# Kernel optimization log

Measured on AMD Instinct MI355X. Metric: run time of the kernel, lower is better.

Reference implementation:

```python
import jax, jax.numpy as jnp
from jax import lax
import numpy as np

N_ATOMS, N_BONDS, N_GRAPHS = 8192, 32768, 256
EMBED, HIDDEN, DEPTH = 32, 256, 10
ATOM_VOCAB, BOND_VOCAB = 200, 10


def setup_inputs() -> dict:
    key = jax.random.key(0)
    ks = jax.random.split(key, 16)
    f = lambda k, *sh: jax.random.normal(k, sh, dtype=jnp.float32) * 0.05
    return {
        "atom_features": jax.random.randint(ks[0], (N_ATOMS,), 0, ATOM_VOCAB),
        "bond_features": jax.random.randint(ks[1], (N_BONDS,), 0, BOND_VOCAB),
        "adjacency_matrix": jax.random.randint(ks[2], (N_ATOMS, N_ATOMS), 0, 2, dtype=jnp.int32),
        "batch_indices": jax.random.randint(ks[3], (N_ATOMS,), 0, N_GRAPHS),
        "atom_emb": f(ks[4], ATOM_VOCAB, EMBED),
        "bond_emb": f(ks[5], BOND_VOCAB, EMBED),
        "msg_W": f(ks[6], DEPTH, HIDDEN, 2 * EMBED),
        "msg_b": f(ks[7], DEPTH, HIDDEN),
        "gru_Wih": f(ks[8], DEPTH, 3 * EMBED, HIDDEN),
        "gru_Whh": f(ks[9], DEPTH, 3 * EMBED, EMBED),
        "gru_bih": f(ks[10], DEPTH, 3 * EMBED),
        "gru_bhh": f(ks[11], DEPTH, 3 * EMBED),
        "pool_W": f(ks[12], HIDDEN, EMBED),
        "pool_b": f(ks[13], HIDDEN),
    }


def _gmpn(atom_emb, bond_emb, msg_W, msg_b, gru_Wih, gru_Whh, gru_bih, gru_bhh,
          pool_W, pool_b, atom_features, bond_features, adjacency_matrix, batch_indices):
    H = atom_emb[atom_features]                       # [N, E]
    A = (adjacency_matrix > 0).astype(H.dtype)        # [N, N] 0/1
    deg = A.sum(axis=1)                               # [N]
    has_nb = deg > 0
    inv_deg = jnp.where(has_nb, 1.0 / jnp.maximum(deg, 1.0), 0.0)[:, None]

    def layer(h, params):
        W, b, wih, whh, b_ih, b_hh = params
        # mean_j Linear([h_i ; h_j]) = W1 h_i + W2 mean_j h_j + b
        neigh_mean = (A @ h) * inv_deg                # [N, E]
        W1, W2 = W[:, :EMBED], W[:, EMBED:]
        msg = h @ W1.T + neigh_mean @ W2.T + b        # [N, HIDDEN]
        msg = jnp.where(has_nb[:, None], msg, 0.0)    # zero message if no neighbors
        # single-step GRU: input=msg, hidden state=h
        gi = msg @ wih.T + b_ih
        gh = h @ whh.T + b_hh
        ir, iz, inn = jnp.split(gi, 3, axis=-1)
        hr, hz, hn = jnp.split(gh, 3, axis=-1)
        r = jax.nn.sigmoid(ir + hr)
        z = jax.nn.sigmoid(iz + hz)
        n = jnp.tanh(inn + r * hn)
        h_new = (1.0 - z) * n + z * h                 # [N, E]
        return h_new, None

    H, _ = lax.scan(layer, H, (msg_W, msg_b, gru_Wih, gru_Whh, gru_bih, gru_bhh))

    # per-graph mean pooling (zeros for empty graphs), then global_pool linear
    seg_sum = jax.ops.segment_sum(H, batch_indices, num_segments=N_GRAPHS)
    cnt = jax.ops.segment_sum(jnp.ones((H.shape[0],), H.dtype), batch_indices, num_segments=N_GRAPHS)
    graph_mean = jnp.where(cnt[:, None] > 0, seg_sum / jnp.maximum(cnt, 1.0)[:, None], 0.0)
    graph_embeddings = graph_mean @ pool_W.T + pool_b  # [G, HIDDEN]

    bond_embeddings = bond_emb[bond_features]          # [B, E]
    return H, bond_embeddings, graph_embeddings


def reference(atom_features, bond_features, adjacency_matrix, batch_indices,
              atom_emb, bond_emb, msg_W, msg_b, gru_Wih, gru_Whh, gru_bih, gru_bhh,
              pool_W, pool_b):
    return _gmpn(atom_emb, bond_emb, msg_W, msg_b, gru_Wih, gru_Whh, gru_bih, gru_bhh,
                 pool_W, pool_b, atom_features, bond_features, adjacency_matrix, batch_indices)
```

## Files before the change

### kernel.cpp

```cpp
#include <hip/hip_runtime.h>
#include <stdint.h>

typedef __bf16 bf16x8 __attribute__((ext_vector_type(8)));
typedef float f32x4 __attribute__((ext_vector_type(4)));

__device__ __forceinline__ float b2f(unsigned short u){
  unsigned int t = ((unsigned int)u) << 16;
  return __builtin_bit_cast(float, t);
}
__device__ __forceinline__ unsigned short f2b(float f){
  unsigned int x = __builtin_bit_cast(unsigned int, f);
  x = x + 0x7FFFu + ((x >> 16) & 1u);
  return (unsigned short)(x >> 16);
}
__device__ __forceinline__ void spread8(unsigned int B, unsigned int w[4]){
  unsigned int m = __umul24(B, 0x8001u);
  w[0] = __umul24(m & 0x00010001u, 0x3F80u);
  w[1] = __umul24(m & 0x00040004u, 0x0FE0u);
  w[2] = __umul24(m & 0x00100010u, 0x03F8u);
  w[3] = __umul24(m & 0x00400040u, 0x00FEu);
}
__device__ __forceinline__ float fsig(float x){ return 1.f/(1.f + __expf(-x)); }
__device__ __forceinline__ float ftanh(float x){ return 1.f - 2.f/(__expf(2.f*x) + 1.f); }

__global__ void k_prep(const void* s_msgW, const void* s_msgb, const void* s_wih,
                       const void* s_whh, const void* s_bih, const void* s_bhh,
                       const void* s_poolW, const void* s_poolb,
                       const unsigned short* __restrict__ aemb_u16,
                       unsigned short* __restrict__ cw,
                       int* __restrict__ deg, float* __restrict__ seg,
                       float* __restrict__ cnt, int* __restrict__ flag){
  int b = blockIdx.x, t = threadIdx.x;
  unsigned int uu = aemb_u16[2*t];
  int e = (int)((uu >> 7) & 0xFF);
  unsigned long long vote = __ballot(e >= 100 && e <= 127);
  int isb = (__popcll(vote) > 32) ? 1 : 0;
  if (b < 1771){
    int id = b*256 + t;
    if (id < 453248){
      const void* src; int off;
      if      (id < 163840){ src = s_msgW;  off = id; }
      else if (id < 166400){ src = s_msgb;  off = id - 163840; }
      else if (id < 412160){ src = s_wih;   off = id - 166400; }
      else if (id < 442880){ src = s_whh;   off = id - 412160; }
      else if (id < 443840){ src = s_bih;   off = id - 442880; }
      else if (id < 444800){ src = s_bhh;   off = id - 443840; }
      else if (id < 452992){ src = s_poolW; off = id - 444800; }
      else                 { src = s_poolb; off = id - 452992; }
      cw[id] = isb ? ((const unsigned short*)src)[off]
                   : f2b(((const float*)src)[off]);
    }
  } else {
    int id2 = (b - 1771)*256 + t;
    if (id2 < 8192){ deg[id2] = 0; seg[id2] = 0.f; }
    if (id2 < 256) cnt[id2] = 0.f;
    if (b == 1771 && t == 0) flag[0] = isb;
  }
}

__global__ void k_pack(const int* __restrict__ adj, unsigned int* __restrict__ mask3,
                       int* __restrict__ deg){
  int tid = blockIdx.x*256 + threadIdx.x;
  int rb  = tid >> 12;
  int rem = tid & 4095;
  int kgg = rem >> 6;
  int L   = rem & 63;
  int lc = L & 15, q = L >> 4;
  int row = rb*16 + lc;
  const int* arow = adj + (size_t)row*8192 + kgg*128 + q*8;
  unsigned int dw = 0; int pc = 0;
  #pragma unroll
  for (int s=0;s<4;s++){
    const int* p = arow + s*32;
    unsigned int b = 0;
    #pragma unroll
    for (int t=0;t<8;t++) b |= (p[t] > 0 ? 1u : 0u) << t;
    dw |= b << (8*s);
    pc += __popc(b);
  }
  mask3[tid] = dw;
  pc += __shfl_xor(pc, 16);
  pc += __shfl_xor(pc, 32);
  if (q == 0) atomicAdd(deg + row, pc);
}

__global__ void k_bond(const int* __restrict__ bft, const void* __restrict__ braw,
                       const int* __restrict__ flag,
                       unsigned short* __restrict__ outB16, float* __restrict__ outB32){
  int id = blockIdx.x*256 + threadIdx.x;
  int e = id >> 5, c = id & 31;
  int idx = bft[e]*32 + c;
  if (flag[0]) outB16[id] = ((const unsigned short*)braw)[idx];
  else         outB32[id] = ((const float*)braw)[idx];
}

__global__ void k_embed(const int* __restrict__ af, const void* __restrict__ araw,
                        const int* __restrict__ flag,
                        float* __restrict__ hf32, uint4* __restrict__ hfrag){
  __shared__ __align__(16) float sh[512];
  int t = threadIdx.x;
  int r = t >> 5, c = t & 31;
  int row = blockIdx.x*16 + r;
  int idx = af[row]*32 + c;
  float f;
  if (flag[0]) f = b2f(((const unsigned short*)araw)[idx]);
  else         f = ((const float*)araw)[idx];
  hf32[row*32 + c] = f;
  sh[r*32 + c] = f;
  __syncthreads();
  if (t < 64){
    int nt = t >> 5, Lq = t & 31;
    int ks32 = blockIdx.x >> 1, half = blockIdx.x & 1;
    int col = nt*16 + (Lq & 15);
    int rbase = (Lq >> 4)*8;
    unsigned int w[4];
    #pragma unroll
    for (int p=0;p<4;p++){
      unsigned int lo = f2b(sh[(rbase + 2*p    )*32 + col]);
      unsigned int hi = f2b(sh[(rbase + 2*p + 1)*32 + col]);
      w[p] = lo | (hi << 16);
    }
    hfrag[(ks32*2 + nt)*64 + half*32 + Lq] = make_uint4(w[0],w[1],w[2],w[3]);
  }
}

__launch_bounds__(512)
__global__ void k_layer(const unsigned int* __restrict__ mask3,
                        const uint4* __restrict__ hfragIn,
                        unsigned int* __restrict__ hfragOut,
                        float* __restrict__ hf32,
                        const int* __restrict__ deg,
                        const unsigned short* __restrict__ msgW,
                        const unsigned short* __restrict__ msgb,
                        const unsigned short* __restrict__ wih,
                        const unsigned short* __restrict__ whh,
                        const unsigned short* __restrict__ bih,
                        const unsigned short* __restrict__ bhh,
                        const int* __restrict__ bidx,
                        float* __restrict__ seg, float* __restrict__ cnt,
                        unsigned short* __restrict__ out16, float* __restrict__ out32,
                        const int* __restrict__ flag, int last)
{
  __shared__ __align__(16) char uni[33792];
  __shared__ __align__(16) unsigned short sA[32][72];
  __shared__ __align__(16) unsigned short smsg[32][264];
  __shared__ int sdeg[32];

  const int t = threadIdx.x;
  const int b = blockIdx.x;
  const int w = t >> 6, L = t & 63;
  const int q = L >> 4, lc = L & 15;
  const int rowbase = b*32;

  const int r0 = t >> 4;
  const int cl = t & 15;
  const int r  = rowbase + r0;
  const int isb = flag[0];
  const int dgr = deg[r];
  const float invr = dgr > 0 ? 1.f/(float)dgr : 0.f;
  float h0 = hf32[r*32 + cl];
  float h1 = hf32[r*32 + 16 + cl];
  sA[r0][cl]    = f2b(h0);
  sA[r0][16+cl] = f2b(h1);
  if (cl == 0) sdeg[r0] = dgr;

  {
    f32x4 a00={0,0,0,0}, a01={0,0,0,0}, a10={0,0,0,0}, a11={0,0,0,0};
    const unsigned int* mp = mask3 + (size_t)b*8192 + w*512 + L;
    const uint4* bp = hfragIn + (size_t)w*4096 + L;
    for (int g=0; g<8; g++){
      unsigned int mw0 = mp[g*64];
      unsigned int mw1 = mp[4096 + g*64];
      #pragma unroll
      for (int s=0; s<4; s++){
        int ks = g*4 + s;
        uint4 u0 = bp[ks*128];
        uint4 u1 = bp[ks*128 + 64];
        union { unsigned int u[4]; bf16x8 v; } A0, A1, B0, B1;
        spread8((mw0 >> (8*s)) & 0xFFu, A0.u);
        spread8((mw1 >> (8*s)) & 0xFFu, A1.u);
        B0.u[0]=u0.x; B0.u[1]=u0.y; B0.u[2]=u0.z; B0.u[3]=u0.w;
        B1.u[0]=u1.x; B1.u[1]=u1.y; B1.u[2]=u1.z; B1.u[3]=u1.w;
        a00 = __builtin_amdgcn_mfma_f32_16x16x32_bf16(A0.v, B0.v, a00, 0,0,0);
        a01 = __builtin_amdgcn_mfma_f32_16x16x32_bf16(A0.v, B1.v, a01, 0,0,0);
        a10 = __builtin_amdgcn_mfma_f32_16x16x32_bf16(A1.v, B0.v, a10, 0,0,0);
        a11 = __builtin_amdgcn_mfma_f32_16x16x32_bf16(A1.v, B1.v, a11, 0,0,0);
      }
    }
    float* sp = (float*)uni + w*1056;
    #pragma unroll
    for (int rg=0; rg<4; rg++){
      int rw = q*4 + rg;
      sp[rw*33 + lc]         = a00[rg];
      sp[rw*33 + 16 + lc]    = a01[rg];
      sp[(16+rw)*33 + lc]    = a10[rg];
      sp[(16+rw)*33 + 16+lc] = a11[rg];
    }
  }
  __syncthreads();
  {
    const float* spf = (const float*)uni;
    float s0 = 0.f, s1 = 0.f;
    #pragma unroll
    for (int ww=0; ww<8; ww++){
      s0 += spf[ww*1056 + r0*33 + cl];
      s1 += spf[ww*1056 + r0*33 + 16 + cl];
    }
    sA[r0][32+cl] = f2b(s0*invr);
    sA[r0][48+cl] = f2b(s1*invr);
  }
  __syncthreads();
  {
    int rt = w & 1, ntb = (w >> 1)*4;
    union { uint4 u; bf16x8 v; } A0, A1;
    A0.u = *(const uint4*)&sA[rt*16 + lc][q*8];
    A1.u = *(const uint4*)&sA[rt*16 + lc][32 + q*8];
    #pragma unroll
    for (int i=0; i<4; i++){
      int nt = ntb + i;
      union { uint4 u; bf16x8 v; } B0, B1;
      B0.u = *(const uint4*)(msgW + (size_t)(nt*16 + lc)*64 + q*8);
      B1.u = *(const uint4*)(msgW + (size_t)(nt*16 + lc)*64 + 32 + q*8);
      f32x4 am = {0,0,0,0};
      am = __builtin_amdgcn_mfma_f32_16x16x32_bf16(A0.v, B0.v, am, 0,0,0);
      am = __builtin_amdgcn_mfma_f32_16x16x32_bf16(A1.v, B1.v, am, 0,0,0);
      float bv = b2f(msgb[nt*16 + lc]);
      #pragma unroll
      for (int rg=0; rg<4; rg++){
        int rw = rt*16 + q*4 + rg;
        float v = am[rg] + bv;
        if (sdeg[rw] == 0) v = 0.f;
        smsg[rw][nt*16 + lc] = f2b(v);
      }
    }
  }
  __syncthreads();
  {
    float* sgi = (float*)uni;
    float* sgh = (float*)(uni + 12800);
    if (w < 6){
      int nt = w;
      f32x4 g0 = {0,0,0,0}, g1 = {0,0,0,0};
      #pragma unroll
      for (int ks=0; ks<8; ks++){
        union { uint4 u; bf16x8 v; } A0, A1, B;
        B.u  = *(const uint4*)(wih + (size_t)(nt*16 + lc)*256 + ks*32 + q*8);
        A0.u = *(const uint4*)&smsg[lc][ks*32 + q*8];
        A1.u = *(const uint4*)&smsg[16 + lc][ks*32 + q*8];
        g0 = __builtin_amdgcn_mfma_f32_16x16x32_bf16(A0.v, B.v, g0, 0,0,0);
        g1 = __builtin_amdgcn_mfma_f32_16x16x32_bf16(A1.v, B.v, g1, 0,0,0);
      }
      #pragma unroll
      for (int rg=0; rg<4; rg++){
        sgi[(q*4+rg)*100      + nt*16 + lc] = g0[rg];
        sgi[(16+q*4+rg)*100   + nt*16 + lc] = g1[rg];
      }
    } else {
      int rt = w - 6;
      union { uint4 u; bf16x8 v; } A;
      A.u = *(const uint4*)&sA[rt*16 + lc][q*8];
      #pragma unroll
      for (int nt=0; nt<6; nt++){
        union { uint4 u; bf16x8 v; } B;
        B.u = *(const uint4*)(whh + (size_t)(nt*16 + lc)*32 + q*8);
        f32x4 hh = {0,0,0,0};
        hh = __builtin_amdgcn_mfma_f32_16x16x32_bf16(A.v, B.v, hh, 0,0,0);
        #pragma unroll
        for (int rg=0; rg<4; rg++)
          sgh[(rt*16 + q*4+rg)*100 + nt*16 + lc] = hh[rg];
      }
    }
  }
  __syncthreads();
  {
    const float* sgi = (const float*)uni;
    const float* sgh = (const float*)(uni + 12800);
    float ir0 = sgi[r0*100 + cl]    + b2f(bih[cl]),    hr0 = sgh[r0*100 + cl]    + b2f(bhh[cl]);
    float iz0 = sgi[r0*100 + 32+cl] + b2f(bih[32+cl]), hz0 = sgh[r0*100 + 32+cl] + b2f(bhh[32+cl]);
    float in0 = sgi[r0*100 + 64+cl] + b2f(bih[64+cl]), hn0 = sgh[r0*100 + 64+cl] + b2f(bhh[64+cl]);
    float ir1 = sgi[r0*100 + 16+cl] + b2f(bih[16+cl]), hr1 = sgh[r0*100 + 16+cl] + b2f(bhh[16+cl]);
    float iz1 = sgi[r0*100 + 48+cl] + b2f(bih[48+cl]), hz1 = sgh[r0*100 + 48+cl] + b2f(bhh[48+cl]);
    float in1 = sgi[r0*100 + 80+cl] + b2f(bih[80+cl]), hn1 = sgh[r0*100 + 80+cl] + b2f(bhh[80+cl]);
    float rr0 = fsig(ir0 + hr0), zz0 = fsig(iz0 + hz0);
    float rr1 = fsig(ir1 + hr1), zz1 = fsig(iz1 + hz1);
    float nn0 = ftanh(in0 + rr0*hn0);
    float nn1 = ftanh(in1 + rr1*hn1);
    h0 = (1.f - zz0)*nn0 + zz0*h0;
    h1 = (1.f - zz1)*nn1 + zz1*h1;
    hf32[r*32 + cl]      = h0;
    hf32[r*32 + 16 + cl] = h1;
    unsigned int m0 = f2b(h0), m1 = f2b(h1);
    unsigned int p0 = (unsigned int)__shfl_xor((int)m0, 16);
    unsigned int p1 = (unsigned int)__shfl_xor((int)m1, 16);
    if ((r & 1) == 0){
      int ks32 = r >> 5;
      int Lf = ((r >> 3) & 3)*16 + cl;
      int pidx = (r & 7) >> 1;
      hfragOut[((ks32*2 + 0)*64 + Lf)*4 + pidx] = m0 | (p0 << 16);
      hfragOut[((ks32*2 + 1)*64 + Lf)*4 + pidx] = m1 | (p1 << 16);
    }
    if (last){
      if (isb){ out16[r*32 + cl] = (unsigned short)m0; out16[r*32 + 16 + cl] = (unsigned short)m1; }
      else    { out32[r*32 + cl] = h0; out32[r*32 + 16 + cl] = h1; }
      int gb = bidx[r];
      atomicAdd(seg + gb*32 + cl, h0);
      atomicAdd(seg + gb*32 + 16 + cl, h1);
      if (cl == 0) atomicAdd(cnt + gb, 1.f);
    }
  }
}

__global__ void k_pool(const float* __restrict__ seg, const float* __restrict__ cnt,
                       const unsigned short* __restrict__ pw, const unsigned short* __restrict__ pb,
                       const int* __restrict__ flag,
                       unsigned short* __restrict__ outG16, float* __restrict__ outG32){
  int g = blockIdx.x, o = threadIdx.x;
  float cv = cnt[g];
  float ic = cv > 0.f ? 1.f/cv : 0.f;
  float s = 0.f;
  #pragma unroll
  for (int c=0;c<32;c++) s += seg[g*32+c]*ic*b2f(pw[o*32+c]);
  s += b2f(pb[o]);
  if (flag[0]) outG16[g*256 + o] = f2b(s);
  else         outG32[g*256 + o] = s;
}

extern "C" void kernel_launch(void* const* d_in, const int* in_sizes, int n_in,
                              void* d_out, int out_size, void* d_ws, size_t ws_size,
                              hipStream_t stream){
  const int* af   = (const int*)d_in[0];
  const int* bft  = (const int*)d_in[1];
  const int* adj  = (const int*)d_in[2];
  const int* bidx = (const int*)d_in[3];

  char* ws = (char*)d_ws;
  unsigned int*   mask3  = (unsigned int*)(ws + 0);
  unsigned int*   hfrag0 = (unsigned int*)(ws + 8388608);
  unsigned int*   hfrag1 = (unsigned int*)(ws + 8912896);
  float*          hf32   = (float*)(ws + 9437184);
  int*            deg    = (int*)(ws + 10485760);
  float*          seg    = (float*)(ws + 10518528);
  float*          cnt    = (float*)(ws + 10551296);
  int*            flag   = (int*)(ws + 10552320);
  unsigned short* cw     = (unsigned short*)(ws + 10552384);

  unsigned short* o16 = (unsigned short*)d_out;
  float*          o32 = (float*)d_out;

  k_prep<<<1803, 256, 0, stream>>>(d_in[6], d_in[7], d_in[8], d_in[9], d_in[10],
                                   d_in[11], d_in[12], d_in[13],
                                   (const unsigned short*)d_in[4],
                                   cw, deg, seg, cnt, flag);
  k_pack<<<8192, 256, 0, stream>>>(adj, mask3, deg);
  k_bond<<<4096, 256, 0, stream>>>(bft, d_in[5], flag, o16 + 262144, o32 + 262144);
  k_embed<<<512, 512, 0, stream>>>(af, d_in[4], flag, hf32, (uint4*)hfrag0);

  for (int d = 0; d < 10; d++){
    const uint4*  hin  = (const uint4*)((d & 1) ? hfrag1 : hfrag0);
    unsigned int* hout = (d & 1) ? hfrag0 : hfrag1;
    k_layer<<<256, 512, 0, stream>>>(mask3, hin, hout, hf32, deg,
                                     cw + (size_t)d*16384,        cw + 163840 + d*256,
                                     cw + 166400 + (size_t)d*24576, cw + 412160 + d*3072,
                                     cw + 442880 + d*96,          cw + 443840 + d*96,
                                     bidx, seg, cnt, o16, o32, flag, (d == 9) ? 1 : 0);
  }
  k_pool<<<256, 256, 0, stream>>>(seg, cnt, cw + 444800, cw + 452992, flag,
                                  o16 + 1310720, o32 + 1310720);
}
```

Baseline: 535.3 us.

## Stage layer weights into swizzled LDS asynchronously and double-buffer neighbor loads

The layer kernel now copies the message, GRU input and hidden weights plus biases into a swizzled LDS region with global_load_lds. The copy is issued before the neighbor aggregation, so the later GEMMs read weights from LDS instead of global memory. The aggregation loop is software-pipelined with two register buffers of mask words and h fragments, and the adjacency packing kernel uses int4 vector loads. The kernels also gain launch_bounds(512,2), but roughly 150KB of LDS per block likely prevents two blocks per CU, and the larger register use and LDS footprint could lower occupancy.

```diff
diff --git a/kernel.cpp b/kernel.cpp
--- a/kernel.cpp
+++ b/kernel.cpp
@@ -22,6 +22,29 @@
 }
 __device__ __forceinline__ float fsig(float x){ return 1.f/(1.f + __expf(-x)); }
 __device__ __forceinline__ float ftanh(float x){ return 1.f - 2.f/(__expf(2.f*x) + 1.f); }
+
+__device__ __forceinline__ void gload_lds16(const void* gsrc, void* ldst){
+  __builtin_amdgcn_global_load_lds(
+      (const __attribute__((address_space(1))) unsigned int*)gsrc,
+      (__attribute__((address_space(3))) unsigned int*)ldst,
+      16, 0, 0);
+}
+
+__device__ __forceinline__ const char* stage_src(int s,
+    const char* mW, const char* wi, const char* wh,
+    const char* mb, const char* bi, const char* bh){
+  if (s >= 5664) s = 5600;
+  int o = s*16;
+  if (o < 32768){ int a = o ^ ((((unsigned)o>>7)&7)<<4); return mW + a; }
+  if (o < 81920){ int a = o - 32768; a ^= (((unsigned)a>>9)&7)<<4; return wi + a; }
+  if (o < 89600){ int a = o - 81920; int row = a/80; int col = a - row*80;
+                  if (col >= 64) col = 0; return wh + row*64 + col; }
+  int a = o - 89600;
+  if (a < 512)  return mb + a;
+  if (a < 704)  return bi + (a - 512);
+  if (a < 896)  return bh + (a - 704);
+  return mb;
+}
 
 __global__ void k_prep(const void* s_msgW, const void* s_msgb, const void* s_wih,
                        const void* s_whh, const void* s_bih, const void* s_bhh,
@@ -67,14 +90,20 @@
   int L   = rem & 63;
   int lc = L & 15, q = L >> 4;
   int row = rb*16 + lc;
-  const int* arow = adj + (size_t)row*8192 + kgg*128 + q*8;
+  const int4* p4 = (const int4*)(adj + (size_t)row*8192 + kgg*128 + q*8);
   unsigned int dw = 0; int pc = 0;
   #pragma unroll
   for (int s=0;s<4;s++){
-    const int* p = arow + s*32;
-    unsigned int b = 0;
-    #pragma unroll
-    for (int t=0;t<8;t++) b |= (p[t] > 0 ? 1u : 0u) << t;
+    int4 u = p4[s*8];
+    int4 v = p4[s*8 + 1];
+    unsigned int b = (unsigned int)(u.x > 0)
+                   | ((unsigned int)(u.y > 0) << 1)
+                   | ((unsigned int)(u.z > 0) << 2)
+                   | ((unsigned int)(u.w > 0) << 3)
+                   | ((unsigned int)(v.x > 0) << 4)
+                   | ((unsigned int)(v.y > 0) << 5)
+                   | ((unsigned int)(v.z > 0) << 6)
+                   | ((unsigned int)(v.w > 0) << 7);
     dw |= b << (8*s);
     pc += __popc(b);
   }
@@ -124,7 +153,21 @@
   }
 }
 
-__launch_bounds__(512)
+#define NEIGH_STEP(MW0, MW1, P0, P1)                                        \
+  _Pragma("unroll")                                                         \
+  for (int s=0; s<4; s++){                                                  \
+    union { unsigned int u[4]; bf16x8 v; } A0, A1, B0, B1;                  \
+    spread8((MW0 >> (8*s)) & 0xFFu, A0.u);                                  \
+    spread8((MW1 >> (8*s)) & 0xFFu, A1.u);                                  \
+    B0.u[0]=P0[s].x; B0.u[1]=P0[s].y; B0.u[2]=P0[s].z; B0.u[3]=P0[s].w;     \
+    B1.u[0]=P1[s].x; B1.u[1]=P1[s].y; B1.u[2]=P1[s].z; B1.u[3]=P1[s].w;     \
+    a00 = __builtin_amdgcn_mfma_f32_16x16x32_bf16(A0.v, B0.v, a00, 0,0,0);  \
+    a01 = __builtin_amdgcn_mfma_f32_16x16x32_bf16(A0.v, B1.v, a01, 0,0,0);  \
+    a10 = __builtin_amdgcn_mfma_f32_16x16x32_bf16(A1.v, B0.v, a10, 0,0,0);  \
+    a11 = __builtin_amdgcn_mfma_f32_16x16x32_bf16(A1.v, B1.v, a11, 0,0,0);  \
+  }
+
+__launch_bounds__(512, 2)
 __global__ void k_layer(const unsigned int* __restrict__ mask3,
                         const uint4* __restrict__ hfragIn,
                         unsigned int* __restrict__ hfragOut,
@@ -144,6 +187,7 @@
   __shared__ __align__(16) char uni[33792];
   __shared__ __align__(16) unsigned short sA[32][72];
   __shared__ __align__(16) unsigned short smsg[32][264];
+  __shared__ __align__(16) char wlds[91136];
   __shared__ int sdeg[32];
 
   const int t = threadIdx.x;
@@ -168,25 +212,50 @@
     f32x4 a00={0,0,0,0}, a01={0,0,0,0}, a10={0,0,0,0}, a11={0,0,0,0};
     const unsigned int* mp = mask3 + (size_t)b*8192 + w*512 + L;
     const uint4* bp = hfragIn + (size_t)w*4096 + L;
-    for (int g=0; g<8; g++){
-      unsigned int mw0 = mp[g*64];
-      unsigned int mw1 = mp[4096 + g*64];
+
+    uint4 pa0[4], pa1[4], pb0[4], pb1[4];
+    unsigned int ma0, ma1, mb0, mb1;
+    ma0 = mp[0];  ma1 = mp[4096];
+    mb0 = mp[64]; mb1 = mp[4096 + 64];
+    #pragma unroll
+    for (int s=0;s<4;s++){ pa0[s]=bp[s*128];     pa1[s]=bp[s*128 + 64]; }
+    #pragma unroll
+    for (int s=0;s<4;s++){ pb0[s]=bp[(4+s)*128]; pb1[s]=bp[(4+s)*128 + 64]; }
+
+    {
+      const char* mW = (const char*)msgW;
+      const char* wi = (const char*)wih;
+      const char* wh = (const char*)whh;
+      const char* mb = (const char*)msgb;
+      const char* bi = (const char*)bih;
+      const char* bh = (const char*)bhh;
       #pragma unroll
-      for (int s=0; s<4; s++){
-        int ks = g*4 + s;
-        uint4 u0 = bp[ks*128];
-        uint4 u1 = bp[ks*128 + 64];
-        union { unsigned int u[4]; bf16x8 v; } A0, A1, B0, B1;
-        spread8((mw0 >> (8*s)) & 0xFFu, A0.u);
-        spread8((mw1 >> (8*s)) & 0xFFu, A1.u);
-        B0.u[0]=u0.x; B0.u[1]=u0.y; B0.u[2]=u0.z; B0.u[3]=u0.w;
-        B1.u[0]=u1.x; B1.u[1]=u1.y; B1.u[2]=u1.z; B1.u[3]=u1.w;
-        a00 = __builtin_amdgcn_mfma_f32_16x16x32_bf16(A0.v, B0.v, a00, 0,0,0);
-        a01 = __builtin_amdgcn_mfma_f32_16x16x32_bf16(A0.v, B1.v, a01, 0,0,0);
-        a10 = __builtin_amdgcn_mfma_f32_16x16x32_bf16(A1.v, B0.v, a10, 0,0,0);
-        a11 = __builtin_amdgcn_mfma_f32_16x16x32_bf16(A1.v, B1.v, a11, 0,0,0);
-      }
-    }
+      for (int it=0; it<12; ++it){
+        int base = it*512 + w*64;
+        if (base < 5696){
+          int s = base + L;
+          const char* src = stage_src(s, mW, wi, wh, mb, bi, bh);
+          gload_lds16(src, wlds + (size_t)base*16 + (size_t)L*16);
+        }
+      }
+    }
+
+    #pragma unroll
+    for (int g=0; g<8; g+=2){
+      NEIGH_STEP(ma0, ma1, pa0, pa1);
+      if (g+2 < 8){
+        ma0 = mp[(g+2)*64]; ma1 = mp[4096 + (g+2)*64];
+        #pragma unroll
+        for (int s=0;s<4;s++){ int ks=(g+2)*4+s; pa0[s]=bp[ks*128]; pa1[s]=bp[ks*128+64]; }
+      }
+      NEIGH_STEP(mb0, mb1, pb0, pb1);
+      if (g+3 < 8){
+        mb0 = mp[(g+3)*64]; mb1 = mp[4096 + (g+3)*64];
+        #pragma unroll
+        for (int s=0;s<4;s++){ int ks=(g+3)*4+s; pb0[s]=bp[ks*128]; pb1[s]=bp[ks*128+64]; }
+      }
+    }
+
     float* sp = (float*)uni + w*1056;
     #pragma unroll
     for (int rg=0; rg<4; rg++){
@@ -212,19 +281,21 @@
   __syncthreads();
   {
     int rt = w & 1, ntb = (w >> 1)*4;
+    int sw = (lc & 7) << 4;
     union { uint4 u; bf16x8 v; } A0, A1;
     A0.u = *(const uint4*)&sA[rt*16 + lc][q*8];
     A1.u = *(const uint4*)&sA[rt*16 + lc][32 + q*8];
     #pragma unroll
     for (int i=0; i<4; i++){
       int nt = ntb + i;
+      int abase = (nt*16 + lc)*128 + q*16;
       union { uint4 u; bf16x8 v; } B0, B1;
-      B0.u = *(const uint4*)(msgW + (size_t)(nt*16 + lc)*64 + q*8);
-      B1.u = *(const uint4*)(msgW + (size_t)(nt*16 + lc)*64 + 32 + q*8);
+      B0.u = *(const uint4*)(wlds + ((abase     ) ^ sw));
+      B1.u = *(const uint4*)(wlds + ((abase + 64) ^ sw));
       f32x4 am = {0,0,0,0};
       am = __builtin_amdgcn_mfma_f32_16x16x32_bf16(A0.v, B0.v, am, 0,0,0);
       am = __builtin_amdgcn_mfma_f32_16x16x32_bf16(A1.v, B1.v, am, 0,0,0);
-      float bv = b2f(msgb[nt*16 + lc]);
+      float bv = b2f(*(const unsigned short*)(wlds + 89600 + (nt*16 + lc)*2));
       #pragma unroll
       for (int rg=0; rg<4; rg++){
         int rw = rt*16 + q*4 + rg;
@@ -240,11 +311,13 @@
     float* sgh = (float*)(uni + 12800);
     if (w < 6){
       int nt = w;
+      int sw = (lc & 7) << 4;
       f32x4 g0 = {0,0,0,0}, g1 = {0,0,0,0};
       #pragma unroll
       for (int ks=0; ks<8; ks++){
         union { uint4 u; bf16x8 v; } A0, A1, B;
-        B.u  = *(const uint4*)(wih + (size_t)(nt*16 + lc)*256 + ks*32 + q*8);
+        int al = (nt*16 + lc)*512 + ks*64 + q*16;
+        B.u  = *(const uint4*)(wlds + 32768 + (al ^ sw));
         A0.u = *(const uint4*)&smsg[lc][ks*32 + q*8];
         A1.u = *(const uint4*)&smsg[16 + lc][ks*32 + q*8];
         g0 = __builtin_amdgcn_mfma_f32_16x16x32_bf16(A0.v, B.v, g0, 0,0,0);
@@ -262,7 +335,7 @@
       #pragma unroll
       for (int nt=0; nt<6; nt++){
         union { uint4 u; bf16x8 v; } B;
-        B.u = *(const uint4*)(whh + (size_t)(nt*16 + lc)*32 + q*8);
+        B.u = *(const uint4*)(wlds + 81920 + (nt*16 + lc)*80 + q*16);
         f32x4 hh = {0,0,0,0};
         hh = __builtin_amdgcn_mfma_f32_16x16x32_bf16(A.v, B.v, hh, 0,0,0);
         #pragma unroll
@@ -275,12 +348,14 @@
   {
     const float* sgi = (const float*)uni;
     const float* sgh = (const float*)(uni + 12800);
-    float ir0 = sgi[r0*100 + cl]    + b2f(bih[cl]),    hr0 = sgh[r0*100 + cl]    + b2f(bhh[cl]);
-    float iz0 = sgi[r0*100 + 32+cl] + b2f(bih[32+cl]), hz0 = sgh[r0*100 + 32+cl] + b2f(bhh[32+cl]);
-    float in0 = sgi[r0*100 + 64+cl] + b2f(bih[64+cl]), hn0 = sgh[r0*100 + 64+cl] + b2f(bhh[64+cl]);
-    float ir1 = sgi[r0*100 + 16+cl] + b2f(bih[16+cl]), hr1 = sgh[r0*100 + 16+cl] + b2f(bhh[16+cl]);
-    float iz1 = sgi[r0*100 + 48+cl] + b2f(bih[48+cl]), hz1 = sgh[r0*100 + 48+cl] + b2f(bhh[48+cl]);
-    float in1 = sgi[r0*100 + 80+cl] + b2f(bih[80+cl]), hn1 = sgh[r0*100 + 80+cl] + b2f(bhh[80+cl]);
+    const unsigned short* bihL = (const unsigned short*)(wlds + 90112);
+    const unsigned short* bhhL = (const unsigned short*)(wlds + 90304);
+    float ir0 = sgi[r0*100 + cl]    + b2f(bihL[cl]),    hr0 = sgh[r0*100 + cl]    + b2f(bhhL[cl]);
+    float iz0 = sgi[r0*100 + 32+cl] + b2f(bihL[32+cl]), hz0 = sgh[r0*100 + 32+cl] + b2f(bhhL[32+cl]);
+    float in0 = sgi[r0*100 + 64+cl] + b2f(bihL[64+cl]), hn0 = sgh[r0*100 + 64+cl] + b2f(bhhL[64+cl]);
+    float ir1 = sgi[r0*100 + 16+cl] + b2f(bihL[16+cl]), hr1 = sgh[r0*100 + 16+cl] + b2f(bhhL[16+cl]);
+    float iz1 = sgi[r0*100 + 48+cl] + b2f(bihL[48+cl]), hz1 = sgh[r0*100 + 48+cl] + b2f(bhhL[48+cl]);
+    float in1 = sgi[r0*100 + 80+cl] + b2f(bihL[80+cl]), hn1 = sgh[r0*100 + 80+cl] + b2f(bhhL[80+cl]);
     float rr0 = fsig(ir0 + hr0), zz0 = fsig(iz0 + hz0);
     float rr1 = fsig(ir1 + hr1), zz1 = fsig(iz1 + hz1);
     float nn0 = ftanh(in0 + rr0*hn0);
```

Result: no change. 536.1 us (+0.1%).
